# Optimization experiments

Measured on AMD Instinct MI355X. Metric: run time of the kernel, lower is better.

The kernel has to match this reference:

```python
import jax, jax.numpy as jnp
import numpy as np

B, N, K, LEN_INIT = 4, 4096, 10, 3
LEN_INPUT = 3 * (K + 1) + 3 * K + LEN_INIT  # 66


def setup_inputs() -> dict:
    key = jax.random.key(0)
    ks = jax.random.split(key, 6)
    return {
        "position": jax.random.normal(ks[0], (B, N, 3), dtype=jnp.float32),
        "velocity": jax.random.normal(ks[1], (B, N, 3), dtype=jnp.float32),
        "init_config": jax.random.normal(ks[2], (B, LEN_INIT), dtype=jnp.float32),
        "W1": jax.random.normal(ks[3], (32, LEN_INPUT), dtype=jnp.float32) * 0.1,
        "b1": jnp.zeros((32,), dtype=jnp.float32),
        "W2": jax.random.normal(ks[4], (16, 32), dtype=jnp.float32) * 0.1,
        "b2": jnp.zeros((16,), dtype=jnp.float32),
        "W3": jax.random.normal(ks[5], (6, 16), dtype=jnp.float32) * 0.1,
        "b3": jnp.zeros((6,), dtype=jnp.float32),
    }


def reference(position, velocity, init_config, W1, b1, W2, b2, W3, b3):
    Bc, Nc, _ = position.shape
    # pairwise squared distances [B,N,N]; same topk ordering as euclidean cdist
    sq = jnp.sum(position * position, axis=-1)  # [B,N]
    d2 = sq[:, :, None] + sq[:, None, :] - 2.0 * jnp.einsum("bnd,bmd->bnm", position, position)
    # k+1 nearest (including self), ascending distance
    _, nn_idx = jax.lax.top_k(-d2, K + 1)  # [B,N,K+1]
    # gather neighbor features per batch element
    vel_nn = jax.vmap(lambda v, i: v[i])(velocity, nn_idx)          # [B,N,K+1,3]
    pos_nn = jax.vmap(lambda p, i: p[i])(position, nn_idx[:, :, 1:])  # [B,N,K,3]
    pos_off = pos_nn - position[:, :, None, :]  # relative positions, no self
    feats = jnp.concatenate(
        [
            pos_off.reshape(Bc, Nc, 3 * K),
            vel_nn.reshape(Bc, Nc, 3 * (K + 1)),
            jnp.broadcast_to(init_config[:, None, :], (Bc, Nc, LEN_INIT)),
        ],
        axis=2,
    )  # [B,N,66]
    # three stacked linear layers (no nonlinearity, matching nn.Sequential of Linears)
    h = feats @ W1.T + b1
    h = h @ W2.T + b2
    pred = h @ W3.T + b3  # [B,N,6]
    return pred.at[:, :, :3].add(position)
```

## Files before the change

### kernel.cpp

```cpp
#include <hip/hip_runtime.h>
#include <stdint.h>

#define BATCH 4
#define NPTS 4096
#define KNN 11
#define LPQ 16
#define QPB 16
#define CHUNK 1024
#define NCHUNK (NPTS / CHUNK)
#define CPL (CHUNK / LPQ)
#define BUFN 10
#define SENT_BITS 0x433FFFFFFFFFFFFFll

__device__ __forceinline__ unsigned sortable_f32(float d) {
    unsigned b = __float_as_uint(d);
    unsigned m = (unsigned)(((int)b) >> 31) | 0x80000000u;
    return b ^ m;
}

__global__ __launch_bounds__(256, 4) void fused_kernel(
    const float* __restrict__ pos, const float* __restrict__ vel,
    const float* __restrict__ initc,
    const float* __restrict__ W1, const float* __restrict__ b1,
    const float* __restrict__ W2, const float* __restrict__ b2,
    const float* __restrict__ W3, const float* __restrict__ b3,
    float* __restrict__ out)
{
#pragma clang fp contract(off)
    __shared__ float4 sp[CHUNK + LPQ];
    __shared__ unsigned long long buf[BUFN * 256];

    int b    = blockIdx.x >> 8;
    int qblk = blockIdx.x & 255;
    int tid  = threadIdx.x;
    const float* pb = pos + (size_t)b * NPTS * 3;

    int q = tid >> 4, p = tid & 15;
    int i = qblk * QPB + q;

    float xq = pb[3*i], yq = pb[3*i+1], zq = pb[3*i+2];
    float sqq = xq*xq + yq*yq + zq*zq;

    double kd[KNN];
#pragma unroll
    for (int k = 0; k < KNN; ++k) kd[k] = __longlong_as_double(SENT_BITS);
    float tau_f = __builtin_inff();
    int cnt = 0, nflush = 0;

    for (int c = 0; c < NCHUNK; ++c) {
        if (c) __syncthreads();
        for (int j = tid; j < CHUNK; j += 256) {
            int g = c * CHUNK + j;
            float x = pb[3*g], y = pb[3*g+1], z = pb[3*g+2];
            float sq = x*x + y*y + z*z;
            sp[j + (j >> 6)] = make_float4(x, y, z, sq);
        }
        __syncthreads();

        int sbase = p * (CPL + 1);
        int jg    = c * CHUNK + p * CPL;
        for (int jl = 0; jl < CPL; jl += 4) {
            float4 c0 = sp[sbase + jl + 0];
            float4 c1 = sp[sbase + jl + 1];
            float4 c2 = sp[sbase + jl + 2];
            float4 c3 = sp[sbase + jl + 3];
            float t0 = xq*c0.x, t1 = xq*c1.x, t2 = xq*c2.x, t3 = xq*c3.x;
            t0 = fmaf(yq, c0.y, t0); t1 = fmaf(yq, c1.y, t1);
            t2 = fmaf(yq, c2.y, t2); t3 = fmaf(yq, c3.y, t3);
            t0 = fmaf(zq, c0.z, t0); t1 = fmaf(zq, c1.z, t1);
            t2 = fmaf(zq, c2.z, t2); t3 = fmaf(zq, c3.z, t3);
            float d0 = (sqq + c0.w) - 2.0f*t0;
            float d1 = (sqq + c1.w) - 2.0f*t1;
            float d2 = (sqq + c2.w) - 2.0f*t2;
            float d3 = (sqq + c3.w) - 2.0f*t3;

#pragma unroll
            for (int s = 0; s < 4; ++s) {
                float dv = s == 0 ? d0 : s == 1 ? d1 : s == 2 ? d2 : d3;
                if (dv <= tau_f) {
                    unsigned u  = sortable_f32(dv);
                    unsigned lo = (u << 12) | (unsigned)(jg + jl + s);
                    unsigned hi = 0x43300000u | (u >> 20);
                    buf[cnt * 256 + tid] =
                        ((unsigned long long)hi << 32) | (unsigned long long)lo;
                    ++cnt;
                }
            }

            if (__any(cnt > BUFN - 4)) {
                for (int k = 0; k < BUFN; ++k) {
                    if (!__any(cnt > k)) break;
                    unsigned long long kb = buf[k * 256 + tid];
                    double key = (k < cnt) ? __longlong_as_double(kb)
                                           : __longlong_as_double(SENT_BITS);
#pragma unroll
                    for (int kk = KNN-1; kk > 0; --kk) {
                        double mn = fmin(kd[kk], key);
                        kd[kk] = fmax(kd[kk-1], mn);
                    }
                    kd[0] = fmin(kd[0], key);
                }
                cnt = 0;
                if (nflush < 3) {
                    ++nflush;
                    double tmp[KNN];
#pragma unroll
                    for (int k = 0; k < KNN; ++k) tmp[k] = kd[k];
                    double h = tmp[0];
#pragma unroll
                    for (int r = 0; r < KNN; ++r) {
                        h = tmp[0];
#pragma unroll
                        for (int m = 1; m <= 8; m <<= 1)
                            h = fmin(h, __shfl_xor(h, m, LPQ));
                        bool own = (__double_as_longlong(tmp[0]) ==
                                    __double_as_longlong(h));
#pragma unroll
                        for (int t2 = 0; t2 < KNN-1; ++t2)
                            tmp[t2] = own ? tmp[t2+1] : tmp[t2];
                        tmp[KNN-1] = own ? __longlong_as_double(SENT_BITS)
                                         : tmp[KNN-1];
                    }
                    unsigned tau_u = (unsigned)((unsigned long long)
                                                __double_as_longlong(h) >> 12);
                    tau_f = __uint_as_float(tau_u ^ 0x80000000u);
                }
            }
        }
    }

    for (int k = 0; k < BUFN; ++k) {
        if (!__any(cnt > k)) break;
        unsigned long long kb = buf[k * 256 + tid];
        double key = (k < cnt) ? __longlong_as_double(kb)
                               : __longlong_as_double(SENT_BITS);
#pragma unroll
        for (int kk = KNN-1; kk > 0; --kk) {
            double mn = fmin(kd[kk], key);
            kd[kk] = fmax(kd[kk-1], mn);
        }
        kd[0] = fmin(kd[0], key);
    }

    unsigned res[KNN];
#pragma unroll
    for (int r = 0; r < KNN; ++r) {
        double h = kd[0];
#pragma unroll
        for (int m = 1; m <= 8; m <<= 1)
            h = fmin(h, __shfl_xor(h, m, LPQ));
        long long hb = __double_as_longlong(h);
        res[r] = (unsigned)(hb & 0xFFF);
        bool own = (__double_as_longlong(kd[0]) == hb);
#pragma unroll
        for (int t = 0; t < KNN-1; ++t) kd[t] = own ? kd[t+1] : kd[t];
        kd[KNN-1] = own ? __longlong_as_double(SENT_BITS) : kd[KNN-1];
    }

    const float* vb = vel + (size_t)b * NPTS * 3;

    const float* w0 = W1 + (2*p)   * 66;
    const float* w1 = W1 + (2*p+1) * 66;
    float a0 = b1[2*p], a1 = b1[2*p+1];
#pragma unroll
    for (int k = 1; k < KNN; ++k) {
        const float* pn = pb + 3*(int)res[k];
        float dx = pn[0] - xq, dy = pn[1] - yq, dz = pn[2] - zq;
        int ff = 3*(k-1);
        a0 = fmaf(dx, w0[ff+0], a0); a1 = fmaf(dx, w1[ff+0], a1);
        a0 = fmaf(dy, w0[ff+1], a0); a1 = fmaf(dy, w1[ff+1], a1);
        a0 = fmaf(dz, w0[ff+2], a0); a1 = fmaf(dz, w1[ff+2], a1);
    }
#pragma unroll
    for (int k = 0; k < KNN; ++k) {
        const float* vn = vb + 3*(int)res[k];
        int ff = 30 + 3*k;
        a0 = fmaf(vn[0], w0[ff+0], a0); a1 = fmaf(vn[0], w1[ff+0], a1);
        a0 = fmaf(vn[1], w0[ff+1], a0); a1 = fmaf(vn[1], w1[ff+1], a1);
        a0 = fmaf(vn[2], w0[ff+2], a0); a1 = fmaf(vn[2], w1[ff+2], a1);
    }
    float c0i = initc[b*3+0], c1i = initc[b*3+1], c2i = initc[b*3+2];
    a0 = fmaf(c0i, w0[63], a0); a1 = fmaf(c0i, w1[63], a1);
    a0 = fmaf(c1i, w0[64], a0); a1 = fmaf(c1i, w1[64], a1);
    a0 = fmaf(c2i, w0[65], a0); a1 = fmaf(c2i, w1[65], a1);

    float h2 = b2[p];
    const float* w2 = W2 + p * 32;
#pragma unroll
    for (int ii = 0; ii < 32; ++ii) {
        float h1v = __shfl((ii & 1) ? a1 : a0, ii >> 1, LPQ);
        h2 = fmaf(h1v, w2[ii], h2);
    }
    int o3 = p < 6 ? p : 0;
    float po = b3[o3];
    const float* w3 = W3 + o3 * 16;
#pragma unroll
    for (int ii = 0; ii < 16; ++ii) {
        float h2v = __shfl(h2, ii, LPQ);
        po = fmaf(h2v, w3[ii], po);
    }
    float resid = (p == 0) ? xq : (p == 1) ? yq : (p == 2) ? zq : 0.0f;
    po += resid;

    if (p < 6)
        out[((size_t)b * NPTS + (size_t)i) * 6 + p] = po;
}

extern "C" void kernel_launch(void* const* d_in, const int* in_sizes, int n_in,
                              void* d_out, int out_size, void* d_ws, size_t ws_size,
                              hipStream_t stream) {
    const float* pos   = (const float*)d_in[0];
    const float* vel   = (const float*)d_in[1];
    const float* initc = (const float*)d_in[2];
    const float* W1    = (const float*)d_in[3];
    const float* b1    = (const float*)d_in[4];
    const float* W2    = (const float*)d_in[5];
    const float* b2    = (const float*)d_in[6];
    const float* W3    = (const float*)d_in[7];
    const float* b3    = (const float*)d_in[8];
    float* out = (float*)d_out;

    fused_kernel<<<dim3(BATCH * (NPTS / QPB)), dim3(256), 0, stream>>>(
        pos, vel, initc, W1, b1, W2, b2, W3, b3, out);
}
```

Before: 125.7 us.

## Process two queries per thread to reuse shared-memory candidate loads

Each thread now handles two query points, so each block covers 32 queries and the grid is halved. Every float4 candidate read from shared memory is used for two distance computations, halving LDS traffic and the per-chunk staging cost per query. The price is doubled register state for the top-k lists, a second shared buffer, and launch bounds lowered to 2 blocks per CU, which reduces occupancy.

```diff
diff --git a/kernel.cpp b/kernel.cpp
--- a/kernel.cpp
+++ b/kernel.cpp
@@ -5,7 +5,7 @@
 #define NPTS 4096
 #define KNN 11
 #define LPQ 16
-#define QPB 16
+#define QPB 32
 #define CHUNK 1024
 #define NCHUNK (NPTS / CHUNK)
 #define CPL (CHUNK / LPQ)
@@ -18,7 +18,120 @@
     return b ^ m;
 }
 
-__global__ __launch_bounds__(256, 4) void fused_kernel(
+__device__ __forceinline__ void drain_buf(const unsigned long long* buf,
+                                          int tid, int cnt, double* kd) {
+#pragma clang fp contract(off)
+    for (int k = 0; k < BUFN; ++k) {
+        if (!__any(cnt > k)) break;
+        unsigned long long kb = buf[k * 256 + tid];
+        double key = (k < cnt) ? __longlong_as_double(kb)
+                               : __longlong_as_double(SENT_BITS);
+#pragma unroll
+        for (int kk = KNN-1; kk > 0; --kk) {
+            double mn = fmin(kd[kk], key);
+            kd[kk] = fmax(kd[kk-1], mn);
+        }
+        kd[0] = fmin(kd[0], key);
+    }
+}
+
+__device__ __forceinline__ float tau_update(const double* kd) {
+#pragma clang fp contract(off)
+    double tmp[KNN];
+#pragma unroll
+    for (int k = 0; k < KNN; ++k) tmp[k] = kd[k];
+    double h = tmp[0];
+#pragma unroll
+    for (int r = 0; r < KNN; ++r) {
+        h = tmp[0];
+#pragma unroll
+        for (int m = 1; m <= 8; m <<= 1)
+            h = fmin(h, __shfl_xor(h, m, LPQ));
+        bool own = (__double_as_longlong(tmp[0]) ==
+                    __double_as_longlong(h));
+#pragma unroll
+        for (int t2 = 0; t2 < KNN-1; ++t2)
+            tmp[t2] = own ? tmp[t2+1] : tmp[t2];
+        tmp[KNN-1] = own ? __longlong_as_double(SENT_BITS)
+                         : tmp[KNN-1];
+    }
+    unsigned tau_u = (unsigned)((unsigned long long)
+                                __double_as_longlong(h) >> 12);
+    return __uint_as_float(tau_u ^ 0x80000000u);
+}
+
+__device__ __forceinline__ void merge_mlp_store(
+    double* kd, float xq, float yq, float zq,
+    const float* __restrict__ pb, const float* __restrict__ vb,
+    const float* __restrict__ W1, const float* __restrict__ b1,
+    const float* __restrict__ W2, const float* __restrict__ b2,
+    const float* __restrict__ W3, const float* __restrict__ b3,
+    float c0i, float c1i, float c2i,
+    int p, int b, int i, float* __restrict__ out)
+{
+#pragma clang fp contract(off)
+    unsigned res[KNN];
+#pragma unroll
+    for (int r = 0; r < KNN; ++r) {
+        double h = kd[0];
+#pragma unroll
+        for (int m = 1; m <= 8; m <<= 1)
+            h = fmin(h, __shfl_xor(h, m, LPQ));
+        long long hb = __double_as_longlong(h);
+        res[r] = (unsigned)(hb & 0xFFF);
+        bool own = (__double_as_longlong(kd[0]) == hb);
+#pragma unroll
+        for (int t = 0; t < KNN-1; ++t) kd[t] = own ? kd[t+1] : kd[t];
+        kd[KNN-1] = own ? __longlong_as_double(SENT_BITS) : kd[KNN-1];
+    }
+
+    const float* w0 = W1 + (2*p)   * 66;
+    const float* w1 = W1 + (2*p+1) * 66;
+    float a0 = b1[2*p], a1 = b1[2*p+1];
+#pragma unroll
+    for (int k = 1; k < KNN; ++k) {
+        const float* pn = pb + 3*(int)res[k];
+        float dx = pn[0] - xq, dy = pn[1] - yq, dz = pn[2] - zq;
+        int ff = 3*(k-1);
+        a0 = fmaf(dx, w0[ff+0], a0); a1 = fmaf(dx, w1[ff+0], a1);
+        a0 = fmaf(dy, w0[ff+1], a0); a1 = fmaf(dy, w1[ff+1], a1);
+        a0 = fmaf(dz, w0[ff+2], a0); a1 = fmaf(dz, w1[ff+2], a1);
+    }
+#pragma unroll
+    for (int k = 0; k < KNN; ++k) {
+        const float* vn = vb + 3*(int)res[k];
+        int ff = 30 + 3*k;
+        a0 = fmaf(vn[0], w0[ff+0], a0); a1 = fmaf(vn[0], w1[ff+0], a1);
+        a0 = fmaf(vn[1], w0[ff+1], a0); a1 = fmaf(vn[1], w1[ff+1], a1);
+        a0 = fmaf(vn[2], w0[ff+2], a0); a1 = fmaf(vn[2], w1[ff+2], a1);
+    }
+    a0 = fmaf(c0i, w0[63], a0); a1 = fmaf(c0i, w1[63], a1);
+    a0 = fmaf(c1i, w0[64], a0); a1 = fmaf(c1i, w1[64], a1);
+    a0 = fmaf(c2i, w0[65], a0); a1 = fmaf(c2i, w1[65], a1);
+
+    float h2 = b2[p];
+    const float* w2 = W2 + p * 32;
+#pragma unroll
+    for (int ii = 0; ii < 32; ++ii) {
+        float h1v = __shfl((ii & 1) ? a1 : a0, ii >> 1, LPQ);
+        h2 = fmaf(h1v, w2[ii], h2);
+    }
+    int o3 = p < 6 ? p : 0;
+    float po = b3[o3];
+    const float* w3 = W3 + o3 * 16;
+#pragma unroll
+    for (int ii = 0; ii < 16; ++ii) {
+        float h2v = __shfl(h2, ii, LPQ);
+        po = fmaf(h2v, w3[ii], po);
+    }
+    float resid = (p == 0) ? xq : (p == 1) ? yq : (p == 2) ? zq : 0.0f;
+    po += resid;
+
+    if (p < 6)
+        out[((size_t)b * NPTS + (size_t)i) * 6 + p] = po;
+}
+
+__global__ __launch_bounds__(256, 2) void fused_kernel(
     const float* __restrict__ pos, const float* __restrict__ vel,
     const float* __restrict__ initc,
     const float* __restrict__ W1, const float* __restrict__ b1,
@@ -28,24 +141,31 @@
 {
 #pragma clang fp contract(off)
     __shared__ float4 sp[CHUNK + LPQ];
-    __shared__ unsigned long long buf[BUFN * 256];
-
-    int b    = blockIdx.x >> 8;
-    int qblk = blockIdx.x & 255;
+    __shared__ unsigned long long bufA[BUFN * 256];
+    __shared__ unsigned long long bufB[BUFN * 256];
+
+    int b    = blockIdx.x >> 7;
+    int qblk = blockIdx.x & 127;
     int tid  = threadIdx.x;
     const float* pb = pos + (size_t)b * NPTS * 3;
 
     int q = tid >> 4, p = tid & 15;
-    int i = qblk * QPB + q;
-
-    float xq = pb[3*i], yq = pb[3*i+1], zq = pb[3*i+2];
-    float sqq = xq*xq + yq*yq + zq*zq;
-
-    double kd[KNN];
-#pragma unroll
-    for (int k = 0; k < KNN; ++k) kd[k] = __longlong_as_double(SENT_BITS);
-    float tau_f = __builtin_inff();
-    int cnt = 0, nflush = 0;
+    int iA = qblk * QPB + q;
+    int iB = iA + 16;
+
+    float xqA = pb[3*iA], yqA = pb[3*iA+1], zqA = pb[3*iA+2];
+    float sqqA = xqA*xqA + yqA*yqA + zqA*zqA;
+    float xqB = pb[3*iB], yqB = pb[3*iB+1], zqB = pb[3*iB+2];
+    float sqqB = xqB*xqB + yqB*yqB + zqB*zqB;
+
+    double kdA[KNN], kdB[KNN];
+#pragma unroll
+    for (int k = 0; k < KNN; ++k) {
+        kdA[k] = __longlong_as_double(SENT_BITS);
+        kdB[k] = __longlong_as_double(SENT_BITS);
+    }
+    float tauA = __builtin_inff(), tauB = __builtin_inff();
+    int cntA = 0, cntB = 0, nfA = 0, nfB = 0;
 
     for (int c = 0; c < NCHUNK; ++c) {
         if (c) __syncthreads();
@@ -64,146 +184,74 @@
             float4 c1 = sp[sbase + jl + 1];
             float4 c2 = sp[sbase + jl + 2];
             float4 c3 = sp[sbase + jl + 3];
-            float t0 = xq*c0.x, t1 = xq*c1.x, t2 = xq*c2.x, t3 = xq*c3.x;
-            t0 = fmaf(yq, c0.y, t0); t1 = fmaf(yq, c1.y, t1);
-            t2 = fmaf(yq, c2.y, t2); t3 = fmaf(yq, c3.y, t3);
-            t0 = fmaf(zq, c0.z, t0); t1 = fmaf(zq, c1.z, t1);
-            t2 = fmaf(zq, c2.z, t2); t3 = fmaf(zq, c3.z, t3);
-            float d0 = (sqq + c0.w) - 2.0f*t0;
-            float d1 = (sqq + c1.w) - 2.0f*t1;
-            float d2 = (sqq + c2.w) - 2.0f*t2;
-            float d3 = (sqq + c3.w) - 2.0f*t3;
+
+            float tA0 = xqA*c0.x, tA1 = xqA*c1.x, tA2 = xqA*c2.x, tA3 = xqA*c3.x;
+            float tB0 = xqB*c0.x, tB1 = xqB*c1.x, tB2 = xqB*c2.x, tB3 = xqB*c3.x;
+            tA0 = fmaf(yqA, c0.y, tA0); tA1 = fmaf(yqA, c1.y, tA1);
+            tA2 = fmaf(yqA, c2.y, tA2); tA3 = fmaf(yqA, c3.y, tA3);
+            tB0 = fmaf(yqB, c0.y, tB0); tB1 = fmaf(yqB, c1.y, tB1);
+            tB2 = fmaf(yqB, c2.y, tB2); tB3 = fmaf(yqB, c3.y, tB3);
+            tA0 = fmaf(zqA, c0.z, tA0); tA1 = fmaf(zqA, c1.z, tA1);
+            tA2 = fmaf(zqA, c2.z, tA2); tA3 = fmaf(zqA, c3.z, tA3);
+            tB0 = fmaf(zqB, c0.z, tB0); tB1 = fmaf(zqB, c1.z, tB1);
+            tB2 = fmaf(zqB, c2.z, tB2); tB3 = fmaf(zqB, c3.z, tB3);
+            float dA0 = (sqqA + c0.w) - 2.0f*tA0;
+            float dA1 = (sqqA + c1.w) - 2.0f*tA1;
+            float dA2 = (sqqA + c2.w) - 2.0f*tA2;
+            float dA3 = (sqqA + c3.w) - 2.0f*tA3;
+            float dB0 = (sqqB + c0.w) - 2.0f*tB0;
+            float dB1 = (sqqB + c1.w) - 2.0f*tB1;
+            float dB2 = (sqqB + c2.w) - 2.0f*tB2;
+            float dB3 = (sqqB + c3.w) - 2.0f*tB3;
 
 #pragma unroll
             for (int s = 0; s < 4; ++s) {
-                float dv = s == 0 ? d0 : s == 1 ? d1 : s == 2 ? d2 : d3;
-                if (dv <= tau_f) {
-                    unsigned u  = sortable_f32(dv);
+                float dvA = s == 0 ? dA0 : s == 1 ? dA1 : s == 2 ? dA2 : dA3;
+                if (dvA <= tauA) {
+                    unsigned u  = sortable_f32(dvA);
                     unsigned lo = (u << 12) | (unsigned)(jg + jl + s);
                     unsigned hi = 0x43300000u | (u >> 20);
-                    buf[cnt * 256 + tid] =
+                    bufA[cntA * 256 + tid] =
                         ((unsigned long long)hi << 32) | (unsigned long long)lo;
-                    ++cnt;
+                    ++cntA;
+                }
+                float dvB = s == 0 ? dB0 : s == 1 ? dB1 : s == 2 ? dB2 : dB3;
+                if (dvB <= tauB) {
+                    unsigned u  = sortable_f32(dvB);
+                    unsigned lo = (u << 12) | (unsigned)(jg + jl + s);
+                    unsigned hi = 0x43300000u | (u >> 20);
+                    bufB[cntB * 256 + tid] =
+                        ((unsigned long long)hi << 32) | (unsigned long long)lo;
+                    ++cntB;
                 }
             }
 
-            if (__any(cnt > BUFN - 4)) {
-                for (int k = 0; k < BUFN; ++k) {
-                    if (!__any(cnt > k)) break;
-                    unsigned long long kb = buf[k * 256 + tid];
-                    double key = (k < cnt) ? __longlong_as_double(kb)
-                                           : __longlong_as_double(SENT_BITS);
-#pragma unroll
-                    for (int kk = KNN-1; kk > 0; --kk) {
-                        double mn = fmin(kd[kk], key);
-                        kd[kk] = fmax(kd[kk-1], mn);
-                    }
-                    kd[0] = fmin(kd[0], key);
-                }
-                cnt = 0;
-                if (nflush < 3) {
-                    ++nflush;
-                    double tmp[KNN];
-#pragma unroll
-                    for (int k = 0; k < KNN; ++k) tmp[k] = kd[k];
-                    double h = tmp[0];
-#pragma unroll
-                    for (int r = 0; r < KNN; ++r) {
-                        h = tmp[0];
-#pragma unroll
-                        for (int m = 1; m <= 8; m <<= 1)
-                            h = fmin(h, __shfl_xor(h, m, LPQ));
-                        bool own = (__double_as_longlong(tmp[0]) ==
-                                    __double_as_longlong(h));
-#pragma unroll
-                        for (int t2 = 0; t2 < KNN-1; ++t2)
-                            tmp[t2] = own ? tmp[t2+1] : tmp[t2];
-                        tmp[KNN-1] = own ? __longlong_as_double(SENT_BITS)
-                                         : tmp[KNN-1];
-                    }
-                    unsigned tau_u = (unsigned)((unsigned long long)
-                                                __double_as_longlong(h) >> 12);
-                    tau_f = __uint_as_float(tau_u ^ 0x80000000u);
+            int over = (cntA > BUFN - 4) | (cntB > BUFN - 4);
+            if (__any(over)) {
+                if (__any(cntA > BUFN - 4)) {
+                    drain_buf(bufA, tid, cntA, kdA);
+                    cntA = 0;
+                    if (nfA < 3) { ++nfA; tauA = tau_update(kdA); }
+                }
+                if (__any(cntB > BUFN - 4)) {
+                    drain_buf(bufB, tid, cntB, kdB);
+                    cntB = 0;
+                    if (nfB < 3) { ++nfB; tauB = tau_update(kdB); }
                 }
             }
         }
     }
 
-    for (int k = 0; k < BUFN; ++k) {
-        if (!__any(cnt > k)) break;
-        unsigned long long kb = buf[k * 256 + tid];
-        double key = (k < cnt) ? __longlong_as_double(kb)
-                               : __longlong_as_double(SENT_BITS);
-#pragma unroll
-        for (int kk = KNN-1; kk > 0; --kk) {
-            double mn = fmin(kd[kk], key);
-            kd[kk] = fmax(kd[kk-1], mn);
-        }
-        kd[0] = fmin(kd[0], key);
-    }
-
-    unsigned res[KNN];
-#pragma unroll
-    for (int r = 0; r < KNN; ++r) {
-        double h = kd[0];
-#pragma unroll
-        for (int m = 1; m <= 8; m <<= 1)
-            h = fmin(h, __shfl_xor(h, m, LPQ));
-        long long hb = __double_as_longlong(h);
-        res[r] = (unsigned)(hb & 0xFFF);
-        bool own = (__double_as_longlong(kd[0]) == hb);
-#pragma unroll
-        for (int t = 0; t < KNN-1; ++t) kd[t] = own ? kd[t+1] : kd[t];
-        kd[KNN-1] = own ? __longlong_as_double(SENT_BITS) : kd[KNN-1];
-    }
+    drain_buf(bufA, tid, cntA, kdA);
+    drain_buf(bufB, tid, cntB, kdB);
 
     const float* vb = vel + (size_t)b * NPTS * 3;
-
-    const float* w0 = W1 + (2*p)   * 66;
-    const float* w1 = W1 + (2*p+1) * 66;
-    float a0 = b1[2*p], a1 = b1[2*p+1];
-#pragma unroll
-    for (int k = 1; k < KNN; ++k) {
-        const float* pn = pb + 3*(int)res[k];
-        float dx = pn[0] - xq, dy = pn[1] - yq, dz = pn[2] - zq;
-        int ff = 3*(k-1);
-        a0 = fmaf(dx, w0[ff+0], a0); a1 = fmaf(dx, w1[ff+0], a1);
-        a0 = fmaf(dy, w0[ff+1], a0); a1 = fmaf(dy, w1[ff+1], a1);
-        a0 = fmaf(dz, w0[ff+2], a0); a1 = fmaf(dz, w1[ff+2], a1);
-    }
-#pragma unroll
-    for (int k = 0; k < KNN; ++k) {
-        const float* vn = vb + 3*(int)res[k];
-        int ff = 30 + 3*k;
-        a0 = fmaf(vn[0], w0[ff+0], a0); a1 = fmaf(vn[0], w1[ff+0], a1);
-        a0 = fmaf(vn[1], w0[ff+1], a0); a1 = fmaf(vn[1], w1[ff+1], a1);
-        a0 = fmaf(vn[2], w0[ff+2], a0); a1 = fmaf(vn[2], w1[ff+2], a1);
-    }
     float c0i = initc[b*3+0], c1i = initc[b*3+1], c2i = initc[b*3+2];
-    a0 = fmaf(c0i, w0[63], a0); a1 = fmaf(c0i, w1[63], a1);
-    a0 = fmaf(c1i, w0[64], a0); a1 = fmaf(c1i, w1[64], a1);
-    a0 = fmaf(c2i, w0[65], a0); a1 = fmaf(c2i, w1[65], a1);
-
-    float h2 = b2[p];
-    const float* w2 = W2 + p * 32;
-#pragma unroll
-    for (int ii = 0; ii < 32; ++ii) {
-        float h1v = __shfl((ii & 1) ? a1 : a0, ii >> 1, LPQ);
-        h2 = fmaf(h1v, w2[ii], h2);
-    }
-    int o3 = p < 6 ? p : 0;
-    float po = b3[o3];
-    const float* w3 = W3 + o3 * 16;
-#pragma unroll
-    for (int ii = 0; ii < 16; ++ii) {
-        float h2v = __shfl(h2, ii, LPQ);
-        po = fmaf(h2v, w3[ii], po);
-    }
-    float resid = (p == 0) ? xq : (p == 1) ? yq : (p == 2) ? zq : 0.0f;
-    po += resid;
-
-    if (p < 6)
-        out[((size_t)b * NPTS + (size_t)i) * 6 + p] = po;
+
+    merge_mlp_store(kdA, xqA, yqA, zqA, pb, vb, W1, b1, W2, b2, W3, b3,
+                    c0i, c1i, c2i, p, b, iA, out);
+    merge_mlp_store(kdB, xqB, yqB, zqB, pb, vb, W1, b1, W2, b2, W3, b3,
+                    c0i, c1i, c2i, p, b, iB, out);
 }
 
 extern "C" void kernel_launch(void* const* d_in, const int* in_sizes, int n_in,
```

Result: slower. 141.7 us (+12.7%).

## Use 32 lanes per query with smaller chunks and higher occupancy

Applied to the files above, without the earlier changes.

Each query is now split across 32 lanes instead of 16, so a block handles 8 queries and the grid doubles to 2048 blocks. The shared chunk shrinks to 512 points with adjusted padding, the candidate buffer drops to 9 entries, and launch bounds ask for 6 blocks per CU. The aim is more parallelism and occupancy for the distance scan and a simpler first MLP layer with one W1 row per lane. In exchange the cross-lane merges of the top-k lists now take five shuffle stages instead of four, and more lanes carry their own K-entry lists that must be merged. The distance expression is also changed to use an FMA.

```diff
diff --git a/kernel.cpp b/kernel.cpp
--- a/kernel.cpp
+++ b/kernel.cpp
@@ -4,12 +4,12 @@
 #define BATCH 4
 #define NPTS 4096
 #define KNN 11
-#define LPQ 16
-#define QPB 16
-#define CHUNK 1024
+#define LPQ 32
+#define QPB 8
+#define CHUNK 512
 #define NCHUNK (NPTS / CHUNK)
 #define CPL (CHUNK / LPQ)
-#define BUFN 10
+#define BUFN 9
 #define SENT_BITS 0x433FFFFFFFFFFFFFll
 
 __device__ __forceinline__ unsigned sortable_f32(float d) {
@@ -18,7 +18,7 @@
     return b ^ m;
 }
 
-__global__ __launch_bounds__(256, 4) void fused_kernel(
+__global__ __launch_bounds__(256, 6) void fused_kernel(
     const float* __restrict__ pos, const float* __restrict__ vel,
     const float* __restrict__ initc,
     const float* __restrict__ W1, const float* __restrict__ b1,
@@ -27,15 +27,15 @@
     float* __restrict__ out)
 {
 #pragma clang fp contract(off)
-    __shared__ float4 sp[CHUNK + LPQ];
+    __shared__ float4 sp[CHUNK + CHUNK/16];
     __shared__ unsigned long long buf[BUFN * 256];
 
-    int b    = blockIdx.x >> 8;
-    int qblk = blockIdx.x & 255;
+    int b    = blockIdx.x >> 9;
+    int qblk = blockIdx.x & 511;
     int tid  = threadIdx.x;
     const float* pb = pos + (size_t)b * NPTS * 3;
 
-    int q = tid >> 4, p = tid & 15;
+    int q = tid >> 5, p = tid & 31;
     int i = qblk * QPB + q;
 
     float xq = pb[3*i], yq = pb[3*i+1], zq = pb[3*i+2];
@@ -53,7 +53,7 @@
             int g = c * CHUNK + j;
             float x = pb[3*g], y = pb[3*g+1], z = pb[3*g+2];
             float sq = x*x + y*y + z*z;
-            sp[j + (j >> 6)] = make_float4(x, y, z, sq);
+            sp[j + (j >> 4)] = make_float4(x, y, z, sq);
         }
         __syncthreads();
 
@@ -69,10 +69,10 @@
             t2 = fmaf(yq, c2.y, t2); t3 = fmaf(yq, c3.y, t3);
             t0 = fmaf(zq, c0.z, t0); t1 = fmaf(zq, c1.z, t1);
             t2 = fmaf(zq, c2.z, t2); t3 = fmaf(zq, c3.z, t3);
-            float d0 = (sqq + c0.w) - 2.0f*t0;
-            float d1 = (sqq + c1.w) - 2.0f*t1;
-            float d2 = (sqq + c2.w) - 2.0f*t2;
-            float d3 = (sqq + c3.w) - 2.0f*t3;
+            float d0 = fmaf(-2.0f, t0, sqq + c0.w);
+            float d1 = fmaf(-2.0f, t1, sqq + c1.w);
+            float d2 = fmaf(-2.0f, t2, sqq + c2.w);
+            float d3 = fmaf(-2.0f, t3, sqq + c3.w);
 
 #pragma unroll
             for (int s = 0; s < 4; ++s) {
@@ -111,7 +111,7 @@
                     for (int r = 0; r < KNN; ++r) {
                         h = tmp[0];
 #pragma unroll
-                        for (int m = 1; m <= 8; m <<= 1)
+                        for (int m = 1; m <= 16; m <<= 1)
                             h = fmin(h, __shfl_xor(h, m, LPQ));
                         bool own = (__double_as_longlong(tmp[0]) ==
                                     __double_as_longlong(h));
@@ -147,7 +147,7 @@
     for (int r = 0; r < KNN; ++r) {
         double h = kd[0];
 #pragma unroll
-        for (int m = 1; m <= 8; m <<= 1)
+        for (int m = 1; m <= 16; m <<= 1)
             h = fmin(h, __shfl_xor(h, m, LPQ));
         long long hb = __double_as_longlong(h);
         res[r] = (unsigned)(hb & 0xFFF);
@@ -159,36 +159,36 @@
 
     const float* vb = vel + (size_t)b * NPTS * 3;
 
-    const float* w0 = W1 + (2*p)   * 66;
-    const float* w1 = W1 + (2*p+1) * 66;
-    float a0 = b1[2*p], a1 = b1[2*p+1];
+    const float* w0 = W1 + p * 66;
+    float a0 = b1[p];
 #pragma unroll
     for (int k = 1; k < KNN; ++k) {
         const float* pn = pb + 3*(int)res[k];
         float dx = pn[0] - xq, dy = pn[1] - yq, dz = pn[2] - zq;
         int ff = 3*(k-1);
-        a0 = fmaf(dx, w0[ff+0], a0); a1 = fmaf(dx, w1[ff+0], a1);
-        a0 = fmaf(dy, w0[ff+1], a0); a1 = fmaf(dy, w1[ff+1], a1);
-        a0 = fmaf(dz, w0[ff+2], a0); a1 = fmaf(dz, w1[ff+2], a1);
+        a0 = fmaf(dx, w0[ff+0], a0);
+        a0 = fmaf(dy, w0[ff+1], a0);
+        a0 = fmaf(dz, w0[ff+2], a0);
     }
 #pragma unroll
     for (int k = 0; k < KNN; ++k) {
         const float* vn = vb + 3*(int)res[k];
         int ff = 30 + 3*k;
-        a0 = fmaf(vn[0], w0[ff+0], a0); a1 = fmaf(vn[0], w1[ff+0], a1);
-        a0 = fmaf(vn[1], w0[ff+1], a0); a1 = fmaf(vn[1], w1[ff+1], a1);
-        a0 = fmaf(vn[2], w0[ff+2], a0); a1 = fmaf(vn[2], w1[ff+2], a1);
+        a0 = fmaf(vn[0], w0[ff+0], a0);
+        a0 = fmaf(vn[1], w0[ff+1], a0);
+        a0 = fmaf(vn[2], w0[ff+2], a0);
     }
     float c0i = initc[b*3+0], c1i = initc[b*3+1], c2i = initc[b*3+2];
-    a0 = fmaf(c0i, w0[63], a0); a1 = fmaf(c0i, w1[63], a1);
-    a0 = fmaf(c1i, w0[64], a0); a1 = fmaf(c1i, w1[64], a1);
-    a0 = fmaf(c2i, w0[65], a0); a1 = fmaf(c2i, w1[65], a1);
-
-    float h2 = b2[p];
-    const float* w2 = W2 + p * 32;
+    a0 = fmaf(c0i, w0[63], a0);
+    a0 = fmaf(c1i, w0[64], a0);
+    a0 = fmaf(c2i, w0[65], a0);
+
+    int p2 = p & 15;
+    float h2 = b2[p2];
+    const float* w2 = W2 + p2 * 32;
 #pragma unroll
     for (int ii = 0; ii < 32; ++ii) {
-        float h1v = __shfl((ii & 1) ? a1 : a0, ii >> 1, LPQ);
+        float h1v = __shfl(a0, ii, LPQ);
         h2 = fmaf(h1v, w2[ii], h2);
     }
     int o3 = p < 6 ? p : 0;
```

Measured after the change: 154.8 us. 23.2% more time.
